# Kernel tuning notes

Hardware: AMD Instinct MI355X
Metric: run time of the kernel (lower is better)

The kernel has to match this reference:

```python
import jax, jax.numpy as jnp
import numpy as np

EMBED = 1024
HEADS = 16
HEAD_DIM = EMBED // HEADS
BATCH = 8
SEQ = 2048


def setup_inputs() -> dict:
    key = jax.random.key(0)
    ks = jax.random.split(key, 6)
    s = EMBED ** -0.5
    x = jax.random.normal(ks[0], (BATCH, SEQ, EMBED), dtype=jnp.float32)
    # weights stored as (in, out); applied as x @ W (equivalent to torch Linear with W.T)
    Wq = jax.random.normal(ks[1], (EMBED, EMBED), dtype=jnp.float32) * s
    Wk = jax.random.normal(ks[2], (EMBED, EMBED), dtype=jnp.float32) * s
    Wv = jax.random.normal(ks[3], (EMBED, EMBED), dtype=jnp.float32) * s
    Wo = jax.random.normal(ks[4], (EMBED, EMBED), dtype=jnp.float32) * s
    bo = jax.random.normal(ks[5], (EMBED,), dtype=jnp.float32) * 0.01
    return {"x": x, "Wq": Wq, "Wk": Wk, "Wv": Wv, "Wo": Wo, "bo": bo}


def reference(x, Wq, Wk, Wv, Wo, bo):
    N, S, E = x.shape
    H, D = HEADS, HEAD_DIM
    # project and reshape to (N, H, S, D) exactly as the torch code (view + permute)
    q = (x @ Wq).reshape(N, S, H, D).transpose(0, 2, 1, 3)
    k = (x @ Wk).reshape(N, S, H, D).transpose(0, 2, 1, 3)
    v = (x @ Wv).reshape(N, S, H, D).transpose(0, 2, 1, 3)
    # Faithful to source: einsum subscripts applied to ALREADY-PERMUTED tensors,
    # so 'a'/'b' range over heads and 's' over seq -> energy is (N, H, H).
    energy = jnp.einsum('nasd,nbsd->nab', q, k)
    attention = jax.nn.softmax(energy / np.sqrt(D).astype(np.float32), axis=2)
    # second einsum: sum over key-heads (b) and value-heads (h) independently
    out = jnp.einsum('nab,nhsd->nasd', attention, v)  # (N, H, S, D)
    out = out.transpose(0, 2, 1, 3).reshape(N, S, E)
    return out @ Wo + bo
```

## Files before the change

kernel.cpp:

```cpp
#include <hip/hip_runtime.h>
#include <hip/hip_bf16.h>


typedef __attribute__((ext_vector_type(8))) short bf16x8;
typedef __attribute__((ext_vector_type(4))) float f32x4;

__device__ __forceinline__ unsigned short f2bf(float f) {
  unsigned int u = __builtin_bit_cast(unsigned int, f);
  u += 0x7FFFu + ((u >> 16) & 1u);
  return (unsigned short)(u >> 16);
}
__device__ __forceinline__ float bf2f(unsigned short b) {
  unsigned int u = ((unsigned int)b) << 16;
  return __builtin_bit_cast(float, u);
}
__device__ __forceinline__ unsigned int pack2(unsigned short a, unsigned short b) {
  return (unsigned int)a | ((unsigned int)b << 16);
}
__device__ __forceinline__ void split2(float a, float b, unsigned int& hi, unsigned int& lo) {
  unsigned short ha = f2bf(a), hb = f2bf(b);
  hi = pack2(ha, hb);
  lo = pack2(f2bf(a - bf2f(ha)), f2bf(b - bf2f(hb)));
}

__global__ __launch_bounds__(256) void prep(
    const float* __restrict__ Wv, const float* __restrict__ Wo,
    unsigned short* __restrict__ BvTh, unsigned short* __restrict__ BvTl,
    unsigned short* __restrict__ BoTh, unsigned short* __restrict__ BoTl) {
  const int b = blockIdx.x, t = threadIdx.x;
  if (b < 64) {
    const int k = b * 16 + (t >> 4);
    const int sub = (t & 15) << 2;
    float s[4] = {0.f, 0.f, 0.f, 0.f};
#pragma unroll
    for (int h = 0; h < 16; ++h) {
      float4 v = *reinterpret_cast<const float4*>(&Wv[k * 1024 + h * 64 + sub]);
      s[0] += v.x; s[1] += v.y; s[2] += v.z; s[3] += v.w;
    }
#pragma unroll
    for (int j = 0; j < 4; ++j) {
      unsigned short h16 = f2bf(s[j]);
      BvTh[(sub + j) * 1024 + k] = h16;
      BvTl[(sub + j) * 1024 + k] = f2bf(s[j] - bf2f(h16));
    }
  } else {
    const int d = b - 64;
    const int e0 = t << 2;
    float s[4] = {0.f, 0.f, 0.f, 0.f};
#pragma unroll
    for (int h = 0; h < 16; ++h) {
      float4 v = *reinterpret_cast<const float4*>(&Wo[(h * 64 + d) * 1024 + e0]);
      s[0] += v.x; s[1] += v.y; s[2] += v.z; s[3] += v.w;
    }
#pragma unroll
    for (int j = 0; j < 4; ++j) {
      unsigned short h16 = f2bf(s[j]);
      BoTh[(e0 + j) * 64 + d] = h16;
      BoTl[(e0 + j) * 64 + d] = f2bf(s[j] - bf2f(h16));
    }
  }
}

__global__ __launch_bounds__(256) void gemm1(
    const float* __restrict__ x,
    const unsigned short* __restrict__ BvTh, const unsigned short* __restrict__ BvTl,
    unsigned short* __restrict__ tmph, unsigned short* __restrict__ tmpl) {
  __shared__ __align__(16) unsigned short Ah[2][32][72], Al[2][32][72];
  __shared__ __align__(16) unsigned short Bh[2][64][72], Bl[2][64][72];
  const int t = threadIdx.x;
  const int r0 = blockIdx.x * 32;
  const int w = t >> 6, l = t & 63;
  const int wr = (w >> 1) << 4;
  const int wc = (w & 1) << 5;
  const int lr = l & 15, lk = (l >> 4) << 3;
  const int srow = t >> 3, skg = (t & 7) << 3;
  const int bcol = t >> 2, bkg = (t & 3) << 4;

  f32x4 acc[2] = {};

  {
    const float* xp = &x[(r0 + srow) * 1024 + skg];
    float4 v0 = *reinterpret_cast<const float4*>(xp);
    float4 v1 = *reinterpret_cast<const float4*>(xp + 4);
    unsigned int h0, h1, h2, h3, lo0, lo1, lo2, lo3;
    split2(v0.x, v0.y, h0, lo0); split2(v0.z, v0.w, h1, lo1);
    split2(v1.x, v1.y, h2, lo2); split2(v1.z, v1.w, h3, lo3);
    *reinterpret_cast<uint4*>(&Ah[0][srow][skg]) = make_uint4(h0, h1, h2, h3);
    *reinterpret_cast<uint4*>(&Al[0][srow][skg]) = make_uint4(lo0, lo1, lo2, lo3);
    const unsigned short* pbh = &BvTh[bcol * 1024 + bkg];
    const unsigned short* pbl = &BvTl[bcol * 1024 + bkg];
    *reinterpret_cast<uint4*>(&Bh[0][bcol][bkg])     = *reinterpret_cast<const uint4*>(pbh);
    *reinterpret_cast<uint4*>(&Bh[0][bcol][bkg + 8]) = *reinterpret_cast<const uint4*>(pbh + 8);
    *reinterpret_cast<uint4*>(&Bl[0][bcol][bkg])     = *reinterpret_cast<const uint4*>(pbl);
    *reinterpret_cast<uint4*>(&Bl[0][bcol][bkg + 8]) = *reinterpret_cast<const uint4*>(pbl + 8);
  }

  for (int c = 0; c < 16; ++c) {
    const int buf = c & 1;
    __syncthreads();
    float4 v0, v1; uint4 nbh0, nbh1, nbl0, nbl1;
    const bool pf = (c + 1 < 16);
    if (pf) {
      const int kb = (c + 1) * 64;
      const float* xp = &x[(r0 + srow) * 1024 + kb + skg];
      v0 = *reinterpret_cast<const float4*>(xp);
      v1 = *reinterpret_cast<const float4*>(xp + 4);
      const unsigned short* pbh = &BvTh[bcol * 1024 + kb + bkg];
      const unsigned short* pbl = &BvTl[bcol * 1024 + kb + bkg];
      nbh0 = *reinterpret_cast<const uint4*>(pbh);
      nbh1 = *reinterpret_cast<const uint4*>(pbh + 8);
      nbl0 = *reinterpret_cast<const uint4*>(pbl);
      nbl1 = *reinterpret_cast<const uint4*>(pbl + 8);
    }
#pragma unroll
    for (int kk = 0; kk < 64; kk += 32) {
      bf16x8 ah = *reinterpret_cast<const bf16x8*>(&Ah[buf][wr + lr][kk + lk]);
      bf16x8 al = *reinterpret_cast<const bf16x8*>(&Al[buf][wr + lr][kk + lk]);
#pragma unroll
      for (int ct = 0; ct < 2; ++ct) {
        const int col = wc + (ct << 4) + lr;
        bf16x8 bh = *reinterpret_cast<const bf16x8*>(&Bh[buf][col][kk + lk]);
        bf16x8 bl = *reinterpret_cast<const bf16x8*>(&Bl[buf][col][kk + lk]);
        acc[ct] = __builtin_amdgcn_mfma_f32_16x16x32_bf16(ah, bh, acc[ct], 0, 0, 0);
        acc[ct] = __builtin_amdgcn_mfma_f32_16x16x32_bf16(ah, bl, acc[ct], 0, 0, 0);
        acc[ct] = __builtin_amdgcn_mfma_f32_16x16x32_bf16(al, bh, acc[ct], 0, 0, 0);
      }
    }
    if (pf) {
      const int nb = buf ^ 1;
      unsigned int h0, h1, h2, h3, lo0, lo1, lo2, lo3;
      split2(v0.x, v0.y, h0, lo0); split2(v0.z, v0.w, h1, lo1);
      split2(v1.x, v1.y, h2, lo2); split2(v1.z, v1.w, h3, lo3);
      *reinterpret_cast<uint4*>(&Ah[nb][srow][skg]) = make_uint4(h0, h1, h2, h3);
      *reinterpret_cast<uint4*>(&Al[nb][srow][skg]) = make_uint4(lo0, lo1, lo2, lo3);
      *reinterpret_cast<uint4*>(&Bh[nb][bcol][bkg])     = nbh0;
      *reinterpret_cast<uint4*>(&Bh[nb][bcol][bkg + 8]) = nbh1;
      *reinterpret_cast<uint4*>(&Bl[nb][bcol][bkg])     = nbl0;
      *reinterpret_cast<uint4*>(&Bl[nb][bcol][bkg + 8]) = nbl1;
    }
  }

#pragma unroll
  for (int ct = 0; ct < 2; ++ct) {
    const int col = wc + (ct << 4) + lr;
#pragma unroll
    for (int j = 0; j < 4; ++j) {
      const int row = r0 + wr + ((l >> 4) << 2) + j;
      float v = acc[ct][j];
      unsigned short h = f2bf(v);
      tmph[row * 64 + col] = h;
      tmpl[row * 64 + col] = f2bf(v - bf2f(h));
    }
  }
}

__global__ __launch_bounds__(256) void gemm2(
    const unsigned short* __restrict__ tmph, const unsigned short* __restrict__ tmpl,
    const unsigned short* __restrict__ BoTh, const unsigned short* __restrict__ BoTl,
    const float* __restrict__ bo, float* __restrict__ out) {
  __shared__ __align__(16) unsigned short Ah[64][72], Al[64][72];
  __shared__ __align__(16) unsigned short Bh[128][72], Bl[128][72];
  const int t = threadIdx.x;
  const int mb = blockIdx.x >> 3, nb = blockIdx.x & 7;
  const int r0 = mb << 6, c0 = nb << 7;
  {
    const int ar = t >> 2, akg = (t & 3) << 4;
    const unsigned short* p = &tmph[(r0 + ar) * 64 + akg];
    *reinterpret_cast<uint4*>(&Ah[ar][akg])     = *reinterpret_cast<const uint4*>(p);
    *reinterpret_cast<uint4*>(&Ah[ar][akg + 8]) = *reinterpret_cast<const uint4*>(p + 8);
    p = &tmpl[(r0 + ar) * 64 + akg];
    *reinterpret_cast<uint4*>(&Al[ar][akg])     = *reinterpret_cast<const uint4*>(p);
    *reinterpret_cast<uint4*>(&Al[ar][akg + 8]) = *reinterpret_cast<const uint4*>(p + 8);
    const int bc = t >> 1, bkg = (t & 1) << 5;
    p = &BoTh[(c0 + bc) * 64 + bkg];
#pragma unroll
    for (int j = 0; j < 4; ++j)
      *reinterpret_cast<uint4*>(&Bh[bc][bkg + j * 8]) = *reinterpret_cast<const uint4*>(p + j * 8);
    p = &BoTl[(c0 + bc) * 64 + bkg];
#pragma unroll
    for (int j = 0; j < 4; ++j)
      *reinterpret_cast<uint4*>(&Bl[bc][bkg + j * 8]) = *reinterpret_cast<const uint4*>(p + j * 8);
  }
  __syncthreads();
  const int w = t >> 6, l = t & 63;
  const int wr = w << 4;
  const int lr = l & 15, lk = (l >> 4) << 3;
  f32x4 acc[8] = {};
#pragma unroll
  for (int kk = 0; kk < 64; kk += 32) {
    bf16x8 ah = *reinterpret_cast<const bf16x8*>(&Ah[wr + lr][kk + lk]);
    bf16x8 al = *reinterpret_cast<const bf16x8*>(&Al[wr + lr][kk + lk]);
#pragma unroll
    for (int ct = 0; ct < 8; ++ct) {
      bf16x8 bh = *reinterpret_cast<const bf16x8*>(&Bh[(ct << 4) + lr][kk + lk]);
      bf16x8 bl = *reinterpret_cast<const bf16x8*>(&Bl[(ct << 4) + lr][kk + lk]);
      acc[ct] = __builtin_amdgcn_mfma_f32_16x16x32_bf16(ah, bh, acc[ct], 0, 0, 0);
      acc[ct] = __builtin_amdgcn_mfma_f32_16x16x32_bf16(ah, bl, acc[ct], 0, 0, 0);
      acc[ct] = __builtin_amdgcn_mfma_f32_16x16x32_bf16(al, bh, acc[ct], 0, 0, 0);
    }
  }
#pragma unroll
  for (int ct = 0; ct < 8; ++ct) {
    const int col = c0 + (ct << 4) + lr;
    const float bv = bo[col];
#pragma unroll
    for (int j = 0; j < 4; ++j) {
      const int row = r0 + wr + ((l >> 4) << 2) + j;
      out[row * 1024 + col] = acc[ct][j] + bv;
    }
  }
}

extern "C" void kernel_launch(void* const* d_in, const int* in_sizes, int n_in,
                              void* d_out, int out_size, void* d_ws, size_t ws_size,
                              hipStream_t stream) {
  const float* x  = (const float*)d_in[0];
  const float* Wv = (const float*)d_in[3];
  const float* Wo = (const float*)d_in[4];
  const float* bo = (const float*)d_in[5];
  float* out = (float*)d_out;

  unsigned short* BvTh = (unsigned short*)d_ws;
  unsigned short* BvTl = BvTh + 65536;
  unsigned short* BoTh = BvTl + 65536;
  unsigned short* BoTl = BoTh + 65536;
  unsigned short* tmph = BoTl + 65536;
  unsigned short* tmpl = tmph + 1048576;

  prep<<<128, 256, 0, stream>>>(Wv, Wo, BvTh, BvTl, BoTh, BoTl);
  gemm1<<<512, 256, 0, stream>>>(x, BvTh, BvTl, tmph, tmpl);
  gemm2<<<2048, 256, 0, stream>>>(tmph, tmpl, BoTh, BoTl, bo, out);
}
```

Baseline: 153.0 us.

## Pre-swizzle weights into MFMA fragment layout and load B directly to registers

The prep kernel now writes the reduced Wv and Wo weights directly in MFMA B-fragment order, so gemm1 and gemm2 load B operands straight from global memory into registers and skip LDS staging. gemm1 also prefetches x two stages ahead and stages its output through LDS for coalesced 16-byte stores. gemm2 uses fewer, wider blocks that loop over 32 column tiles with double-buffered register prefetch of B and bias. This targets LDS traffic and uncoalesced writes, at the cost of higher register pressure and a more rigid layout coupling between the kernels.

```diff
diff --git a/kernel.cpp b/kernel.cpp
--- a/kernel.cpp
+++ b/kernel.cpp
@@ -22,212 +22,256 @@
   hi = pack2(ha, hb);
   lo = pack2(f2bf(a - bf2f(ha)), f2bf(b - bf2f(hb)));
 }
-
-__global__ __launch_bounds__(256) void prep(
-    const float* __restrict__ Wv, const float* __restrict__ Wo,
-    unsigned short* __restrict__ BvTh, unsigned short* __restrict__ BvTl,
-    unsigned short* __restrict__ BoTh, unsigned short* __restrict__ BoTl) {
+__device__ __forceinline__ bf16x8 asbf(uint4 u) { return __builtin_bit_cast(bf16x8, u); }
+
+__global__ __launch_bounds__(256) void prep(const float* __restrict__ Wv,
+                                            const float* __restrict__ Wo,
+                                            unsigned short* __restrict__ BvF,
+                                            unsigned short* __restrict__ BoF) {
   const int b = blockIdx.x, t = threadIdx.x;
-  if (b < 64) {
-    const int k = b * 16 + (t >> 4);
-    const int sub = (t & 15) << 2;
-    float s[4] = {0.f, 0.f, 0.f, 0.f};
-#pragma unroll
-    for (int h = 0; h < 16; ++h) {
-      float4 v = *reinterpret_cast<const float4*>(&Wv[k * 1024 + h * 64 + sub]);
-      s[0] += v.x; s[1] += v.y; s[2] += v.z; s[3] += v.w;
-    }
+  const int l = t & 63, lr = l & 15, lk = (l >> 4) << 3;
+  if (b < 32) {
+    const int s = b, ctg = t >> 6;
+    const int d = (ctg << 4) + lr;
+    const int k0 = (s << 5) + lk;
+    float sum[8] = {};
+#pragma unroll
+    for (int h = 0; h < 16; ++h)
+#pragma unroll
+      for (int j = 0; j < 8; ++j)
+        sum[j] += Wv[(k0 + j) * 1024 + h * 64 + d];
+    unsigned short hh[8], ll[8];
+#pragma unroll
+    for (int j = 0; j < 8; ++j) {
+      hh[j] = f2bf(sum[j]);
+      ll[j] = f2bf(sum[j] - bf2f(hh[j]));
+    }
+    const int base = ((s * 4 + ctg) * 2) * 64 + l;
+    uint4 uh = make_uint4(pack2(hh[0], hh[1]), pack2(hh[2], hh[3]),
+                          pack2(hh[4], hh[5]), pack2(hh[6], hh[7]));
+    uint4 ul = make_uint4(pack2(ll[0], ll[1]), pack2(ll[2], ll[3]),
+                          pack2(ll[4], ll[5]), pack2(ll[6], ll[7]));
+    ((uint4*)BvF)[base] = uh;
+    ((uint4*)BvF)[base + 64] = ul;
+  } else {
+    const int ctg2 = b - 32;
+    const int kk = t >> 7, jh = (t >> 6) & 1;
+    const int e = (ctg2 << 4) + lr;
+    const int kb = (kk << 5) + lk + (jh << 2);
+    float sum[4] = {};
+#pragma unroll
+    for (int h = 0; h < 16; ++h)
+#pragma unroll
+      for (int j = 0; j < 4; ++j)
+        sum[j] += Wo[(h * 64 + kb + j) * 1024 + e];
+    unsigned short hh[4], ll[4];
 #pragma unroll
     for (int j = 0; j < 4; ++j) {
-      unsigned short h16 = f2bf(s[j]);
-      BvTh[(sub + j) * 1024 + k] = h16;
-      BvTl[(sub + j) * 1024 + k] = f2bf(s[j] - bf2f(h16));
-    }
-  } else {
-    const int d = b - 64;
-    const int e0 = t << 2;
-    float s[4] = {0.f, 0.f, 0.f, 0.f};
-#pragma unroll
-    for (int h = 0; h < 16; ++h) {
-      float4 v = *reinterpret_cast<const float4*>(&Wo[(h * 64 + d) * 1024 + e0]);
-      s[0] += v.x; s[1] += v.y; s[2] += v.z; s[3] += v.w;
-    }
-#pragma unroll
-    for (int j = 0; j < 4; ++j) {
-      unsigned short h16 = f2bf(s[j]);
-      BoTh[(e0 + j) * 64 + d] = h16;
-      BoTl[(e0 + j) * 64 + d] = f2bf(s[j] - bf2f(h16));
-    }
-  }
-}
-
-__global__ __launch_bounds__(256) void gemm1(
-    const float* __restrict__ x,
-    const unsigned short* __restrict__ BvTh, const unsigned short* __restrict__ BvTl,
-    unsigned short* __restrict__ tmph, unsigned short* __restrict__ tmpl) {
-  __shared__ __align__(16) unsigned short Ah[2][32][72], Al[2][32][72];
-  __shared__ __align__(16) unsigned short Bh[2][64][72], Bl[2][64][72];
+      hh[j] = f2bf(sum[j]);
+      ll[j] = f2bf(sum[j] - bf2f(hh[j]));
+    }
+    const int base = ((((ctg2 * 2 + kk) * 2) * 64 + l) << 1) + jh;
+    ((uint2*)BoF)[base] = make_uint2(pack2(hh[0], hh[1]), pack2(hh[2], hh[3]));
+    ((uint2*)BoF)[base + 128] = make_uint2(pack2(ll[0], ll[1]), pack2(ll[2], ll[3]));
+  }
+}
+
+__global__ __launch_bounds__(256) void gemm1(const float* __restrict__ x,
+                                             const unsigned short* __restrict__ BvF,
+                                             unsigned short* __restrict__ tmph,
+                                             unsigned short* __restrict__ tmpl) {
+  __shared__ unsigned short Ah[2][32][72], Al[2][32][72];
   const int t = threadIdx.x;
-  const int r0 = blockIdx.x * 32;
+  const int r0 = blockIdx.x << 5;
   const int w = t >> 6, l = t & 63;
   const int wr = (w >> 1) << 4;
-  const int wc = (w & 1) << 5;
+  const int ctgb = (w & 1) << 1;
   const int lr = l & 15, lk = (l >> 4) << 3;
   const int srow = t >> 3, skg = (t & 7) << 3;
-  const int bcol = t >> 2, bkg = (t & 3) << 4;
-
+  const float* xp = &x[(r0 + srow) * 1024 + skg];
+  const uint4* bp = (const uint4*)BvF;
+
+  float4 xr[2][2];
+  uint4 br[2][8];
   f32x4 acc[2] = {};
 
-  {
-    const float* xp = &x[(r0 + srow) * 1024 + skg];
-    float4 v0 = *reinterpret_cast<const float4*>(xp);
-    float4 v1 = *reinterpret_cast<const float4*>(xp + 4);
-    unsigned int h0, h1, h2, h3, lo0, lo1, lo2, lo3;
-    split2(v0.x, v0.y, h0, lo0); split2(v0.z, v0.w, h1, lo1);
-    split2(v1.x, v1.y, h2, lo2); split2(v1.z, v1.w, h3, lo3);
-    *reinterpret_cast<uint4*>(&Ah[0][srow][skg]) = make_uint4(h0, h1, h2, h3);
-    *reinterpret_cast<uint4*>(&Al[0][srow][skg]) = make_uint4(lo0, lo1, lo2, lo3);
-    const unsigned short* pbh = &BvTh[bcol * 1024 + bkg];
-    const unsigned short* pbl = &BvTl[bcol * 1024 + bkg];
-    *reinterpret_cast<uint4*>(&Bh[0][bcol][bkg])     = *reinterpret_cast<const uint4*>(pbh);
-    *reinterpret_cast<uint4*>(&Bh[0][bcol][bkg + 8]) = *reinterpret_cast<const uint4*>(pbh + 8);
-    *reinterpret_cast<uint4*>(&Bl[0][bcol][bkg])     = *reinterpret_cast<const uint4*>(pbl);
-    *reinterpret_cast<uint4*>(&Bl[0][bcol][bkg + 8]) = *reinterpret_cast<const uint4*>(pbl + 8);
-  }
-
+  xr[0][0] = *(const float4*)(xp);
+  xr[0][1] = *(const float4*)(xp + 4);
+  xr[1][0] = *(const float4*)(xp + 64);
+  xr[1][1] = *(const float4*)(xp + 68);
+#pragma unroll
+  for (int kk = 0; kk < 2; ++kk)
+#pragma unroll
+    for (int ct = 0; ct < 2; ++ct)
+#pragma unroll
+      for (int hl = 0; hl < 2; ++hl)
+        br[0][(kk * 2 + ct) * 2 + hl] =
+            bp[((kk * 4 + ctgb + ct) * 2 + hl) * 64 + l];
+  {
+    unsigned int h0, h1, h2, h3, q0, q1, q2, q3;
+    split2(xr[0][0].x, xr[0][0].y, h0, q0);
+    split2(xr[0][0].z, xr[0][0].w, h1, q1);
+    split2(xr[0][1].x, xr[0][1].y, h2, q2);
+    split2(xr[0][1].z, xr[0][1].w, h3, q3);
+    *(uint4*)&Ah[0][srow][skg] = make_uint4(h0, h1, h2, h3);
+    *(uint4*)&Al[0][srow][skg] = make_uint4(q0, q1, q2, q3);
+  }
+
+#pragma unroll
   for (int c = 0; c < 16; ++c) {
     const int buf = c & 1;
+    if (c + 2 < 16) {
+      const float* xq = xp + (c + 2) * 64;
+      xr[buf][0] = *(const float4*)(xq);
+      xr[buf][1] = *(const float4*)(xq + 4);
+    }
+    if (c + 1 < 16) {
+#pragma unroll
+      for (int kk = 0; kk < 2; ++kk)
+#pragma unroll
+        for (int ct = 0; ct < 2; ++ct)
+#pragma unroll
+          for (int hl = 0; hl < 2; ++hl)
+            br[buf ^ 1][(kk * 2 + ct) * 2 + hl] =
+                bp[((((c + 1) * 2 + kk) * 4 + ctgb + ct) * 2 + hl) * 64 + l];
+    }
     __syncthreads();
-    float4 v0, v1; uint4 nbh0, nbh1, nbl0, nbl1;
-    const bool pf = (c + 1 < 16);
-    if (pf) {
-      const int kb = (c + 1) * 64;
-      const float* xp = &x[(r0 + srow) * 1024 + kb + skg];
-      v0 = *reinterpret_cast<const float4*>(xp);
-      v1 = *reinterpret_cast<const float4*>(xp + 4);
-      const unsigned short* pbh = &BvTh[bcol * 1024 + kb + bkg];
-      const unsigned short* pbl = &BvTl[bcol * 1024 + kb + bkg];
-      nbh0 = *reinterpret_cast<const uint4*>(pbh);
-      nbh1 = *reinterpret_cast<const uint4*>(pbh + 8);
-      nbl0 = *reinterpret_cast<const uint4*>(pbl);
-      nbl1 = *reinterpret_cast<const uint4*>(pbl + 8);
-    }
-#pragma unroll
-    for (int kk = 0; kk < 64; kk += 32) {
-      bf16x8 ah = *reinterpret_cast<const bf16x8*>(&Ah[buf][wr + lr][kk + lk]);
-      bf16x8 al = *reinterpret_cast<const bf16x8*>(&Al[buf][wr + lr][kk + lk]);
+#pragma unroll
+    for (int kk = 0; kk < 2; ++kk) {
+      bf16x8 ah = *(const bf16x8*)&Ah[buf][wr + lr][kk * 32 + lk];
+      bf16x8 al = *(const bf16x8*)&Al[buf][wr + lr][kk * 32 + lk];
 #pragma unroll
       for (int ct = 0; ct < 2; ++ct) {
-        const int col = wc + (ct << 4) + lr;
-        bf16x8 bh = *reinterpret_cast<const bf16x8*>(&Bh[buf][col][kk + lk]);
-        bf16x8 bl = *reinterpret_cast<const bf16x8*>(&Bl[buf][col][kk + lk]);
+        bf16x8 bh = asbf(br[buf][(kk * 2 + ct) * 2 + 0]);
+        bf16x8 bl = asbf(br[buf][(kk * 2 + ct) * 2 + 1]);
         acc[ct] = __builtin_amdgcn_mfma_f32_16x16x32_bf16(ah, bh, acc[ct], 0, 0, 0);
         acc[ct] = __builtin_amdgcn_mfma_f32_16x16x32_bf16(ah, bl, acc[ct], 0, 0, 0);
         acc[ct] = __builtin_amdgcn_mfma_f32_16x16x32_bf16(al, bh, acc[ct], 0, 0, 0);
       }
     }
-    if (pf) {
-      const int nb = buf ^ 1;
-      unsigned int h0, h1, h2, h3, lo0, lo1, lo2, lo3;
-      split2(v0.x, v0.y, h0, lo0); split2(v0.z, v0.w, h1, lo1);
-      split2(v1.x, v1.y, h2, lo2); split2(v1.z, v1.w, h3, lo3);
-      *reinterpret_cast<uint4*>(&Ah[nb][srow][skg]) = make_uint4(h0, h1, h2, h3);
-      *reinterpret_cast<uint4*>(&Al[nb][srow][skg]) = make_uint4(lo0, lo1, lo2, lo3);
-      *reinterpret_cast<uint4*>(&Bh[nb][bcol][bkg])     = nbh0;
-      *reinterpret_cast<uint4*>(&Bh[nb][bcol][bkg + 8]) = nbh1;
-      *reinterpret_cast<uint4*>(&Bl[nb][bcol][bkg])     = nbl0;
-      *reinterpret_cast<uint4*>(&Bl[nb][bcol][bkg + 8]) = nbl1;
-    }
-  }
-
-#pragma unroll
-  for (int ct = 0; ct < 2; ++ct) {
-    const int col = wc + (ct << 4) + lr;
-#pragma unroll
-    for (int j = 0; j < 4; ++j) {
-      const int row = r0 + wr + ((l >> 4) << 2) + j;
-      float v = acc[ct][j];
-      unsigned short h = f2bf(v);
-      tmph[row * 64 + col] = h;
-      tmpl[row * 64 + col] = f2bf(v - bf2f(h));
-    }
-  }
-}
-
-__global__ __launch_bounds__(256) void gemm2(
-    const unsigned short* __restrict__ tmph, const unsigned short* __restrict__ tmpl,
-    const unsigned short* __restrict__ BoTh, const unsigned short* __restrict__ BoTl,
-    const float* __restrict__ bo, float* __restrict__ out) {
-  __shared__ __align__(16) unsigned short Ah[64][72], Al[64][72];
-  __shared__ __align__(16) unsigned short Bh[128][72], Bl[128][72];
+    if (c + 1 < 16) {
+      unsigned int h0, h1, h2, h3, q0, q1, q2, q3;
+      float4 a0 = xr[buf ^ 1][0], a1 = xr[buf ^ 1][1];
+      split2(a0.x, a0.y, h0, q0);
+      split2(a0.z, a0.w, h1, q1);
+      split2(a1.x, a1.y, h2, q2);
+      split2(a1.z, a1.w, h3, q3);
+      *(uint4*)&Ah[buf ^ 1][srow][skg] = make_uint4(h0, h1, h2, h3);
+      *(uint4*)&Al[buf ^ 1][srow][skg] = make_uint4(q0, q1, q2, q3);
+    }
+  }
+
+  __syncthreads();
+  {
+    unsigned short* sh = &Ah[0][0][0];
+    unsigned short* sl = &Al[0][0][0];
+#pragma unroll
+    for (int ct = 0; ct < 2; ++ct) {
+      const int col = ((ctgb + ct) << 4) + lr;
+#pragma unroll
+      for (int j = 0; j < 4; ++j) {
+        const int r = wr + ((l >> 4) << 2) + j;
+        float v = acc[ct][j];
+        unsigned short h = f2bf(v);
+        sh[r * 72 + col] = h;
+        sl[r * 72 + col] = f2bf(v - bf2f(h));
+      }
+    }
+  }
+  __syncthreads();
+  {
+    const int row = t >> 3, kg = (t & 7) << 3;
+    uint4 vh = *(const uint4*)&Ah[0][row][kg];
+    uint4 vl = *(const uint4*)&Al[0][row][kg];
+    *(uint4*)&tmph[(r0 + row) * 64 + kg] = vh;
+    *(uint4*)&tmpl[(r0 + row) * 64 + kg] = vl;
+  }
+}
+
+__global__ __launch_bounds__(256) void gemm2(const unsigned short* __restrict__ tmph,
+                                             const unsigned short* __restrict__ tmpl,
+                                             const unsigned short* __restrict__ BoF,
+                                             const float* __restrict__ bo,
+                                             float* __restrict__ out) {
+  __shared__ unsigned short Ah[64][72], Al[64][72];
   const int t = threadIdx.x;
-  const int mb = blockIdx.x >> 3, nb = blockIdx.x & 7;
-  const int r0 = mb << 6, c0 = nb << 7;
-  {
-    const int ar = t >> 2, akg = (t & 3) << 4;
-    const unsigned short* p = &tmph[(r0 + ar) * 64 + akg];
-    *reinterpret_cast<uint4*>(&Ah[ar][akg])     = *reinterpret_cast<const uint4*>(p);
-    *reinterpret_cast<uint4*>(&Ah[ar][akg + 8]) = *reinterpret_cast<const uint4*>(p + 8);
-    p = &tmpl[(r0 + ar) * 64 + akg];
-    *reinterpret_cast<uint4*>(&Al[ar][akg])     = *reinterpret_cast<const uint4*>(p);
-    *reinterpret_cast<uint4*>(&Al[ar][akg + 8]) = *reinterpret_cast<const uint4*>(p + 8);
-    const int bc = t >> 1, bkg = (t & 1) << 5;
-    p = &BoTh[(c0 + bc) * 64 + bkg];
+  const int mb = blockIdx.x >> 1, nb = blockIdx.x & 1;
+  const int r0 = mb << 6, c0 = nb << 9;
+  const int l = t & 63, lr = l & 15, lk = (l >> 4) << 3;
+  const int wr = (t >> 6) << 4;
+  const uint4* bp = (const uint4*)BoF;
+
+  {
+    const int row = t >> 2, kg = (t & 3) << 4;
+    const uint4* ph = (const uint4*)&tmph[(r0 + row) * 64 + kg];
+    uint4 a0 = ph[0], a1 = ph[1];
+    const uint4* pl4 = (const uint4*)&tmpl[(r0 + row) * 64 + kg];
+    uint4 b0 = pl4[0], b1 = pl4[1];
+    *(uint4*)&Ah[row][kg] = a0;
+    *(uint4*)&Ah[row][kg + 8] = a1;
+    *(uint4*)&Al[row][kg] = b0;
+    *(uint4*)&Al[row][kg + 8] = b1;
+  }
+  uint4 brg[2][4];
+  float bvr[2];
+#pragma unroll
+  for (int kk = 0; kk < 2; ++kk)
+#pragma unroll
+    for (int hl = 0; hl < 2; ++hl)
+      brg[0][kk * 2 + hl] = bp[(((nb * 32) * 2 + kk) * 2 + hl) * 64 + l];
+  bvr[0] = bo[c0 + lr];
+  __syncthreads();
+
+  bf16x8 afh[2], afl[2];
+#pragma unroll
+  for (int kk = 0; kk < 2; ++kk) {
+    afh[kk] = *(const bf16x8*)&Ah[wr + lr][kk * 32 + lk];
+    afl[kk] = *(const bf16x8*)&Al[wr + lr][kk * 32 + lk];
+  }
+
+#pragma unroll
+  for (int ct = 0; ct < 32; ++ct) {
+    if (ct + 1 < 32) {
+#pragma unroll
+      for (int kk = 0; kk < 2; ++kk)
+#pragma unroll
+        for (int hl = 0; hl < 2; ++hl)
+          brg[(ct + 1) & 1][kk * 2 + hl] =
+              bp[(((nb * 32 + ct + 1) * 2 + kk) * 2 + hl) * 64 + l];
+      bvr[(ct + 1) & 1] = bo[c0 + ((ct + 1) << 4) + lr];
+    }
+    f32x4 a = {};
+#pragma unroll
+    for (int kk = 0; kk < 2; ++kk) {
+      bf16x8 bh = asbf(brg[ct & 1][kk * 2 + 0]);
+      bf16x8 bl = asbf(brg[ct & 1][kk * 2 + 1]);
+      a = __builtin_amdgcn_mfma_f32_16x16x32_bf16(afh[kk], bh, a, 0, 0, 0);
+      a = __builtin_amdgcn_mfma_f32_16x16x32_bf16(afh[kk], bl, a, 0, 0, 0);
+      a = __builtin_amdgcn_mfma_f32_16x16x32_bf16(afl[kk], bh, a, 0, 0, 0);
+    }
+    const int col = c0 + (ct << 4) + lr;
+    const float bv = bvr[ct & 1];
 #pragma unroll
     for (int j = 0; j < 4; ++j)
-      *reinterpret_cast<uint4*>(&Bh[bc][bkg + j * 8]) = *reinterpret_cast<const uint4*>(p + j * 8);
-    p = &BoTl[(c0 + bc) * 64 + bkg];
-#pragma unroll
-    for (int j = 0; j < 4; ++j)
-      *reinterpret_cast<uint4*>(&Bl[bc][bkg + j * 8]) = *reinterpret_cast<const uint4*>(p + j * 8);
-  }
-  __syncthreads();
-  const int w = t >> 6, l = t & 63;
-  const int wr = w << 4;
-  const int lr = l & 15, lk = (l >> 4) << 3;
-  f32x4 acc[8] = {};
-#pragma unroll
-  for (int kk = 0; kk < 64; kk += 32) {
-    bf16x8 ah = *reinterpret_cast<const bf16x8*>(&Ah[wr + lr][kk + lk]);
-    bf16x8 al = *reinterpret_cast<const bf16x8*>(&Al[wr + lr][kk + lk]);
-#pragma unroll
-    for (int ct = 0; ct < 8; ++ct) {
-      bf16x8 bh = *reinterpret_cast<const bf16x8*>(&Bh[(ct << 4) + lr][kk + lk]);
-      bf16x8 bl = *reinterpret_cast<const bf16x8*>(&Bl[(ct << 4) + lr][kk + lk]);
-      acc[ct] = __builtin_amdgcn_mfma_f32_16x16x32_bf16(ah, bh, acc[ct], 0, 0, 0);
-      acc[ct] = __builtin_amdgcn_mfma_f32_16x16x32_bf16(ah, bl, acc[ct], 0, 0, 0);
-      acc[ct] = __builtin_amdgcn_mfma_f32_16x16x32_bf16(al, bh, acc[ct], 0, 0, 0);
-    }
-  }
-#pragma unroll
-  for (int ct = 0; ct < 8; ++ct) {
-    const int col = c0 + (ct << 4) + lr;
-    const float bv = bo[col];
-#pragma unroll
-    for (int j = 0; j < 4; ++j) {
-      const int row = r0 + wr + ((l >> 4) << 2) + j;
-      out[row * 1024 + col] = acc[ct][j] + bv;
-    }
+      out[(r0 + wr + ((l >> 4) << 2) + j) * 1024 + col] = a[j] + bv;
   }
 }
 
 extern "C" void kernel_launch(void* const* d_in, const int* in_sizes, int n_in,
                               void* d_out, int out_size, void* d_ws, size_t ws_size,
                               hipStream_t stream) {
-  const float* x  = (const float*)d_in[0];
+  const float* x = (const float*)d_in[0];
   const float* Wv = (const float*)d_in[3];
   const float* Wo = (const float*)d_in[4];
   const float* bo = (const float*)d_in[5];
   float* out = (float*)d_out;
 
-  unsigned short* BvTh = (unsigned short*)d_ws;
-  unsigned short* BvTl = BvTh + 65536;
-  unsigned short* BoTh = BvTl + 65536;
-  unsigned short* BoTl = BoTh + 65536;
-  unsigned short* tmph = BoTl + 65536;
+  unsigned short* BvF = (unsigned short*)d_ws;
+  unsigned short* BoF = BvF + 131072;
+  unsigned short* tmph = BoF + 131072;
   unsigned short* tmpl = tmph + 1048576;
 
-  prep<<<128, 256, 0, stream>>>(Wv, Wo, BvTh, BvTl, BoTh, BoTl);
-  gemm1<<<512, 256, 0, stream>>>(x, BvTh, BvTl, tmph, tmpl);
-  gemm2<<<2048, 256, 0, stream>>>(tmph, tmpl, BoTh, BoTl, bo, out);
-}
+  prep<<<96, 256, 0, stream>>>(Wv, Wo, BvF, BoF);
+  gemm1<<<512, 256, 0, stream>>>(x, BvF, tmph, tmpl);
+  gemm2<<<512, 256, 0, stream>>>(tmph, tmpl, BoF, bo, out);
+}
```

Result: no change. 152.7 us (-0.2%).
